# Performance work log

Hardware: AMD Instinct MI355X
Metric: run time of the kernel (lower is better)

Reference implementation:

```python
import jax, jax.numpy as jnp
import numpy as np

N_PIXELS = 1024 * 1024      # flattened image W*H
N_CLASSES = 100             # logit channels / label vocabulary
N_SEGMENTS = 30             # superpixel_regions


def setup_inputs() -> dict:
    key = jax.random.key(0)
    k1, k2, k3 = jax.random.split(key, 3)
    output = jax.random.normal(k1, (N_PIXELS, N_CLASSES), dtype=jnp.float32)
    target = jax.random.randint(k2, (N_PIXELS,), 0, N_CLASSES, dtype=jnp.int64)
    seg_ids = jax.random.randint(k3, (N_PIXELS,), 0, N_SEGMENTS, dtype=jnp.int32)
    return {"output": output, "target": target, "seg_ids": seg_ids}


def reference(output, target, seg_ids):
    # --- per-superpixel histogram mode-voting relabel ---
    # counts[s, c] = number of pixels in superpixel s currently labeled c.
    counts = jnp.zeros((N_SEGMENTS, N_CLASSES), dtype=jnp.int32)
    counts = counts.at[seg_ids, target].add(1)
    # np.argmax over hist of np.unique-sorted labels == smallest class id among ties,
    # which jnp.argmax over the dense class axis reproduces exactly.
    mode = jnp.argmax(counts, axis=1)              # [S]
    relabeled = mode[seg_ids].astype(target.dtype)  # [N]

    # --- CrossEntropyLoss(output, target): mean NLL of log-softmax ---
    logp = jax.nn.log_softmax(output, axis=-1)                       # [N, C]
    nll = -jnp.take_along_axis(logp, target[:, None], axis=-1)[:, 0]  # [N]
    loss = jnp.mean(nll)
    return loss, relabeled
```

## Files before the change

kernel.cpp:

```cpp
#include <hip/hip_runtime.h>
#include <math.h>

#define NCLASS 100
#define NSEG 30
#define F4_PER_ROW 25
#define ROWS_PER_GRP 16
#define F4_PER_GRP (F4_PER_ROW * ROWS_PER_GRP)

__device__ __forceinline__ float e4(float4 v) {
    return __expf(v.x) + __expf(v.y) + __expf(v.z) + __expf(v.w);
}

__global__ __launch_bounds__(256) void ce_hist_kernel(
    const float* __restrict__ logits,
    const int*   __restrict__ target,
    const int*   __restrict__ seg,
    int N,
    int*    __restrict__ g_counts,
    double* __restrict__ g_loss)
{
    __shared__ int    lds_hist[NSEG * NCLASS];
    __shared__ float  part[4][F4_PER_GRP];
    __shared__ double lds_loss[4];

    for (int i = threadIdx.x; i < NSEG * NCLASS; i += blockDim.x) lds_hist[i] = 0;
    __syncthreads();

    const int lane          = threadIdx.x & 63;
    const int wv            = threadIdx.x >> 6;
    const int sub           = lane & 3;
    const int q             = lane >> 2;
    const int wavesPerBlock = blockDim.x >> 6;
    const int gwave         = blockIdx.x * wavesPerBlock + wv;
    const int totWaves      = gridDim.x * wavesPerBlock;
    const int ngroups       = N >> 4;

    double acc = 0.0;

    for (int grp = gwave; grp < ngroups; grp += totWaves) {
        const int row = grp * ROWS_PER_GRP + q;

        const int t = target[row];
        const int s = seg[row];

        const float4* g4 = (const float4*)logits + (size_t)grp * F4_PER_GRP;
        float4 f0 = g4[lane        ];
        float4 f1 = g4[lane + 64   ];
        float4 f2 = g4[lane + 128  ];
        float4 f3 = g4[lane + 192  ];
        float4 f4v= g4[lane + 256  ];
        float4 f5 = g4[lane + 320  ];

        part[wv][lane      ] = e4(f0);
        part[wv][lane + 64 ] = e4(f1);
        part[wv][lane + 128] = e4(f2);
        part[wv][lane + 192] = e4(f3);
        part[wv][lane + 256] = e4(f4v);
        part[wv][lane + 320] = e4(f5);
        if (lane < 16) {
            float4 f6 = g4[lane + 384];
            part[wv][lane + 384] = e4(f6);
        }

        const int base = F4_PER_ROW * q + sub;
        float e = part[wv][base     ] + part[wv][base + 4 ] + part[wv][base + 8 ]
                + part[wv][base + 12] + part[wv][base + 16] + part[wv][base + 20];
        if (sub == 0) e += part[wv][F4_PER_ROW * q + 24];
        e += __shfl_xor(e, 1);
        e += __shfl_xor(e, 2);

        const float xt = logits[(size_t)row * NCLASS + t];

        if (sub == 0) {
            acc += (double)(__logf(e) - xt);
            atomicAdd(&lds_hist[s * NCLASS + t], 1);
        }
    }

    #pragma unroll
    for (int off = 32; off; off >>= 1) acc += __shfl_xor(acc, off);
    if (lane == 0) lds_loss[wv] = acc;
    __syncthreads();

    if (threadIdx.x == 0) {
        double b = 0.0;
        for (int w = 0; w < wavesPerBlock; ++w) b += lds_loss[w];
        atomicAdd(g_loss, b);
    }
    for (int i = threadIdx.x; i < NSEG * NCLASS; i += blockDim.x) {
        int c = lds_hist[i];
        if (c) atomicAdd(&g_counts[i], c);
    }
}

__global__ void finalize_kernel(
    const int* __restrict__ g_counts,
    const double* __restrict__ g_loss,
    int N,
    int* __restrict__ g_mode,
    float* __restrict__ out_loss)
{
    const int t = threadIdx.x;
    const int s = t >> 3;
    const int j = t & 7;
    if (s < NSEG) {
        int bestKey = -1;
        #pragma unroll
        for (int c = j; c < NCLASS; c += 8) {
            int v = g_counts[s * NCLASS + c];
            int key = (v << 7) | (127 - c);
            bestKey = max(bestKey, key);
        }
        bestKey = max(bestKey, __shfl_xor(bestKey, 1));
        bestKey = max(bestKey, __shfl_xor(bestKey, 2));
        bestKey = max(bestKey, __shfl_xor(bestKey, 4));
        if (j == 0) g_mode[s] = 127 - (bestKey & 127);
    }
    if (t == 0) out_loss[0] = (float)(g_loss[0] / (double)N);
}

__global__ __launch_bounds__(256) void relabel_kernel(
    const int* __restrict__ seg,
    const int* __restrict__ g_mode,
    float* __restrict__ out,
    int N)
{
    __shared__ float mode_f[NSEG];
    for (int i = threadIdx.x; i < NSEG; i += blockDim.x)
        mode_f[i] = (float)g_mode[i];
    __syncthreads();

    int idx    = blockIdx.x * blockDim.x + threadIdx.x;
    int stride = gridDim.x * blockDim.x;
    for (int i = idx; i < N; i += stride)
        out[i] = mode_f[seg[i]];
}

extern "C" void kernel_launch(void* const* d_in, const int* in_sizes, int n_in,
                              void* d_out, int out_size, void* d_ws, size_t ws_size,
                              hipStream_t stream)
{
    const float* logits = (const float*)d_in[0];
    const int*   target = (const int*)d_in[1];
    const int*   seg    = (const int*)d_in[2];
    float* out = (float*)d_out;

    const int N = in_sizes[1];

    double* g_loss   = (double*)d_ws;
    int*    g_counts = (int*)((char*)d_ws + 16);
    int*    g_mode   = (int*)((char*)d_ws + 16 + NSEG * NCLASS * sizeof(int));

    hipMemsetAsync(d_ws, 0, 16 + NSEG * NCLASS * sizeof(int), stream);

    ce_hist_kernel<<<1024, 256, 0, stream>>>(logits, target, seg, N, g_counts, g_loss);
    finalize_kernel<<<1, 256, 0, stream>>>(g_counts, g_loss, N, g_mode, out);
    relabel_kernel<<<1024, 256, 0, stream>>>(seg, g_mode, out + 1, N);
}
```

Measured before the change: 108.7 us.

## Prefetch next row group in registers and replicate global histogram counters

Restructures the main loop so each wave loads the next 16-row group of logits, targets and segment ids into registers while computing the current one. The global histogram is split into several replicas selected by block index, and the finalize kernel sums them, to reduce contention on global atomics. The launch grid is doubled. The prefetch raises register use, which may lower occupancy, and the replicas add a larger memset and extra reads in finalize.

```diff
diff --git a/kernel.cpp b/kernel.cpp
--- a/kernel.cpp
+++ b/kernel.cpp
@@ -11,12 +11,27 @@
     return __expf(v.x) + __expf(v.y) + __expf(v.z) + __expf(v.w);
 }
 
+#define STAGE(F0,F1,F2,F3,F4V,F5,F6,T,S,g)                                  \
+    do {                                                                    \
+        const float4* g4_ = (const float4*)logits + (size_t)(g) * F4_PER_GRP; \
+        F0 = g4_[lane      ];                                               \
+        F1 = g4_[lane + 64 ];                                               \
+        F2 = g4_[lane + 128];                                               \
+        F3 = g4_[lane + 192];                                               \
+        F4V= g4_[lane + 256];                                               \
+        F5 = g4_[lane + 320];                                               \
+        if (lane < 16) F6 = g4_[lane + 384];                                \
+        T = target[(g) * ROWS_PER_GRP + q];                                 \
+        S = seg   [(g) * ROWS_PER_GRP + q];                                 \
+    } while (0)
+
 __global__ __launch_bounds__(256) void ce_hist_kernel(
     const float* __restrict__ logits,
     const int*   __restrict__ target,
     const int*   __restrict__ seg,
     int N,
     int*    __restrict__ g_counts,
+    int n_rep,
     double* __restrict__ g_loss)
 {
     __shared__ int    lds_hist[NSEG * NCLASS];
@@ -36,31 +51,34 @@
     const int ngroups       = N >> 4;
 
     double acc = 0.0;
+    const float NEG = -INFINITY;
 
-    for (int grp = gwave; grp < ngroups; grp += totWaves) {
-        const int row = grp * ROWS_PER_GRP + q;
+    int  gA    = gwave;
+    bool haveA = (gA < ngroups);
 
-        const int t = target[row];
-        const int s = seg[row];
+    float4 A0, A1, A2, A3, A4, A5, A6;
+    A6 = make_float4(NEG, NEG, NEG, NEG);
+    int tA = 0, sA = 0;
+    if (haveA) STAGE(A0, A1, A2, A3, A4, A5, A6, tA, sA, gA);
 
-        const float4* g4 = (const float4*)logits + (size_t)grp * F4_PER_GRP;
-        float4 f0 = g4[lane        ];
-        float4 f1 = g4[lane + 64   ];
-        float4 f2 = g4[lane + 128  ];
-        float4 f3 = g4[lane + 192  ];
-        float4 f4v= g4[lane + 256  ];
-        float4 f5 = g4[lane + 320  ];
+    while (haveA) {
+        const int  gB    = gA + totWaves;
+        const bool haveB = (gB < ngroups);
 
-        part[wv][lane      ] = e4(f0);
-        part[wv][lane + 64 ] = e4(f1);
-        part[wv][lane + 128] = e4(f2);
-        part[wv][lane + 192] = e4(f3);
-        part[wv][lane + 256] = e4(f4v);
-        part[wv][lane + 320] = e4(f5);
-        if (lane < 16) {
-            float4 f6 = g4[lane + 384];
-            part[wv][lane + 384] = e4(f6);
-        }
+        float4 B0, B1, B2, B3, B4, B5, B6;
+        B6 = make_float4(NEG, NEG, NEG, NEG);
+        int tB = 0, sB = 0;
+        if (haveB) STAGE(B0, B1, B2, B3, B4, B5, B6, tB, sB, gB);
+
+        const float xt = logits[(size_t)(gA * ROWS_PER_GRP + q) * NCLASS + tA];
+
+        part[wv][lane      ] = e4(A0);
+        part[wv][lane + 64 ] = e4(A1);
+        part[wv][lane + 128] = e4(A2);
+        part[wv][lane + 192] = e4(A3);
+        part[wv][lane + 256] = e4(A4);
+        part[wv][lane + 320] = e4(A5);
+        if (lane < 16) part[wv][lane + 384] = e4(A6);
 
         const int base = F4_PER_ROW * q + sub;
         float e = part[wv][base     ] + part[wv][base + 4 ] + part[wv][base + 8 ]
@@ -69,12 +87,14 @@
         e += __shfl_xor(e, 1);
         e += __shfl_xor(e, 2);
 
-        const float xt = logits[(size_t)row * NCLASS + t];
-
         if (sub == 0) {
             acc += (double)(__logf(e) - xt);
-            atomicAdd(&lds_hist[s * NCLASS + t], 1);
+            atomicAdd(&lds_hist[sA * NCLASS + tA], 1);
         }
+
+        A0 = B0; A1 = B1; A2 = B2; A3 = B3; A4 = B4; A5 = B5; A6 = B6;
+        tA = tB; sA = sB;
+        gA = gB; haveA = haveB;
     }
 
     #pragma unroll
@@ -87,14 +107,16 @@
         for (int w = 0; w < wavesPerBlock; ++w) b += lds_loss[w];
         atomicAdd(g_loss, b);
     }
+    int* my_counts = g_counts + (size_t)(blockIdx.x & (n_rep - 1)) * (NSEG * NCLASS);
     for (int i = threadIdx.x; i < NSEG * NCLASS; i += blockDim.x) {
         int c = lds_hist[i];
-        if (c) atomicAdd(&g_counts[i], c);
+        if (c) atomicAdd(&my_counts[i], c);
     }
 }
 
 __global__ void finalize_kernel(
     const int* __restrict__ g_counts,
+    int n_rep,
     const double* __restrict__ g_loss,
     int N,
     int* __restrict__ g_mode,
@@ -105,9 +127,10 @@
     const int j = t & 7;
     if (s < NSEG) {
         int bestKey = -1;
-        #pragma unroll
         for (int c = j; c < NCLASS; c += 8) {
-            int v = g_counts[s * NCLASS + c];
+            int v = 0;
+            for (int r = 0; r < n_rep; ++r)
+                v += g_counts[r * (NSEG * NCLASS) + s * NCLASS + c];
             int key = (v << 7) | (127 - c);
             bestKey = max(bestKey, key);
         }
@@ -147,13 +170,17 @@
 
     const int N = in_sizes[1];
 
+    int n_rep = 8;
+    size_t need = 16 + (size_t)n_rep * NSEG * NCLASS * sizeof(int) + 128;
+    if (ws_size < need) n_rep = 1;
+
     double* g_loss   = (double*)d_ws;
     int*    g_counts = (int*)((char*)d_ws + 16);
-    int*    g_mode   = (int*)((char*)d_ws + 16 + NSEG * NCLASS * sizeof(int));
+    int*    g_mode   = (int*)((char*)d_ws + 16 + (size_t)n_rep * NSEG * NCLASS * sizeof(int));
 
-    hipMemsetAsync(d_ws, 0, 16 + NSEG * NCLASS * sizeof(int), stream);
+    hipMemsetAsync(d_ws, 0, 16 + (size_t)n_rep * NSEG * NCLASS * sizeof(int), stream);
 
-    ce_hist_kernel<<<1024, 256, 0, stream>>>(logits, target, seg, N, g_counts, g_loss);
-    finalize_kernel<<<1, 256, 0, stream>>>(g_counts, g_loss, N, g_mode, out);
+    ce_hist_kernel<<<2048, 256, 0, stream>>>(logits, target, seg, N, g_counts, n_rep, g_loss);
+    finalize_kernel<<<1, 256, 0, stream>>>(g_counts, n_rep, g_loss, N, g_mode, out);
     relabel_kernel<<<1024, 256, 0, stream>>>(seg, g_mode, out + 1, N);
 }
```

Measured after the change: 115.0 us. +5.7%, slower.
